# Performance work log

Measured on AMD Instinct MI355X. Metric: run time of the kernel, lower is better.

The kernel has to match this reference:

```python
import jax, jax.numpy as jnp
import numpy as np
import math

B, LA, LB, D, H = 8, 2048, 2048, 512, 512

def setup_inputs() -> dict:
    key = jax.random.key(0)
    ks = jax.random.split(key, 6)
    return {
        "input_a": jax.random.normal(ks[0], (B, LA, D), dtype=jnp.float32),
        "input_b": jax.random.normal(ks[1], (B, LB, D), dtype=jnp.float32),
        "mask_a": jax.random.randint(ks[2], (B, LA), 0, 2, dtype=jnp.int32),
        "mask_b": jax.random.randint(ks[3], (B, LB), 0, 2, dtype=jnp.int32),
        "Wa": jax.random.normal(ks[4], (D, H), dtype=jnp.float32) * (1.0 / math.sqrt(D)),
        "ba": jnp.zeros((H,), dtype=jnp.float32),
        "Wb": jax.random.normal(ks[5], (D, H), dtype=jnp.float32) * (1.0 / math.sqrt(D)),
        "bb": jnp.zeros((H,), dtype=jnp.float32),
    }

def reference(input_a, input_b, mask_a, mask_b, Wa, ba, Wb, bb):
    scale = 1.0 / math.sqrt(D)  # math.sqrt(input_dim_a)
    mapped_a = input_a @ Wa + ba            # [B, La, H]
    mapped_b = input_b @ Wb + bb            # [B, Lb, H]
    # final_mask = (mask_a outer mask_b) == 0
    final_mask = (mask_a[:, :, None] * mask_b[:, None, :]) == 0  # [B, La, Lb]
    scores = jnp.einsum('bih,bjh->bij', mapped_a, mapped_b) * scale
    scores = jnp.where(final_mask, jnp.float32(-1e9), scores)
    # attentions_a = softmax over Lb; attentions_b^T = softmax over La axis
    att_a = jax.nn.softmax(scores, axis=-1)   # [B, La, Lb]
    att_bT = jax.nn.softmax(scores, axis=1)   # [B, La, Lb] (= attentions_b.transpose(1,2))
    output_a = jnp.einsum('bij,bjd->bid', att_bT, input_b)  # [B, La, D]
    output_b = jnp.einsum('bij,bid->bjd', att_a, input_a)   # [B, Lb, D]
    return (output_a + input_a, output_b + input_b)
```

## Files before the change

kernel.cpp:

```cpp
#include <hip/hip_runtime.h>
#include <hip/hip_bf16.h>

#define BATCH 8
#define LSEQ 2048
#define DDIM 512

using f32x4 = __attribute__((ext_vector_type(4))) float;
using s16x8 = __attribute__((ext_vector_type(8))) short;

static __device__ __forceinline__ unsigned short f2b(float f) {
  __hip_bfloat16 h = __float2bfloat16(f);
  return __builtin_bit_cast(unsigned short, h);
}
static __device__ __forceinline__ float b2f(unsigned short u) {
  unsigned int v = ((unsigned int)u) << 16;
  return __builtin_bit_cast(float, v);
}

static __device__ __forceinline__ void gld16(const unsigned short* g, unsigned short* l) {
  __builtin_amdgcn_global_load_lds(
      (__attribute__((address_space(1))) void*)(g),
      (__attribute__((address_space(3))) void*)(l), 16, 0, 0);
}

__device__ __forceinline__ void mfma_kloop(
    const unsigned short* __restrict__ A, const unsigned short* __restrict__ Bt,
    int K, int lda, int ldb, unsigned short* sA, unsigned short* sB,
    int tid, f32x4 acc[4][4]) {
  const int wave = tid >> 6, lane = tid & 63;
  const int wm = (wave >> 1) * 64, wn = (wave & 1) * 64;
  const int lr = lane & 15, lq = lane >> 4;
  const int srow = tid >> 2;
  const int sk = (tid & 3) * 8;
  unsigned short* dA0 = sA + wave * 512;
  unsigned short* dA1 = sA + 2048 + wave * 512;
  unsigned short* dB0 = sB + wave * 512;
  unsigned short* dB1 = sB + 2048 + wave * 512;
  const unsigned short* pa0 = A + (size_t)srow * lda + sk;
  const unsigned short* pa1 = A + (size_t)(srow + 64) * lda + sk;
  const unsigned short* pb0 = Bt + (size_t)srow * ldb + sk;
  const unsigned short* pb1 = Bt + (size_t)(srow + 64) * ldb + sk;
  for (int k0 = 0; k0 < K; k0 += 32) {
    gld16(pa0 + k0, dA0);
    gld16(pa1 + k0, dA1);
    gld16(pb0 + k0, dB0);
    gld16(pb1 + k0, dB1);
    __syncthreads();
    s16x8 af[4], bf[4];
#pragma unroll
    for (int r = 0; r < 4; ++r)
      af[r] = *(const s16x8*)(sA + (wm + r * 16 + lr) * 32 + lq * 8);
#pragma unroll
    for (int c = 0; c < 4; ++c)
      bf[c] = *(const s16x8*)(sB + (wn + c * 16 + lr) * 32 + lq * 8);
#pragma unroll
    for (int r = 0; r < 4; ++r)
#pragma unroll
      for (int c = 0; c < 4; ++c)
        acc[r][c] = __builtin_amdgcn_mfma_f32_16x16x32_bf16(af[r], bf[c], acc[r][c], 0, 0, 0);
    __syncthreads();
  }
}

__global__ __launch_bounds__(256) void k_prep(const float* __restrict__ in_a,
                                              const float* __restrict__ in_b,
                                              const int* __restrict__ ma,
                                              const int* __restrict__ mb,
                                              unsigned short* __restrict__ oa,
                                              unsigned short* __restrict__ ob,
                                              float* __restrict__ Pa,
                                              float* __restrict__ Pb) {
  int z = blockIdx.z;
  const float* in = z ? in_b : in_a;
  const int* mask = z ? mb : ma;
  unsigned short* o16 = z ? ob : oa;
  float* partial = z ? Pb : Pa;
  int b = blockIdx.y;
  int l0 = blockIdx.x * 32;
  __shared__ int sm[32];
  if (threadIdx.x < 32) sm[threadIdx.x] = mask[b * LSEQ + l0 + threadIdx.x];
  __syncthreads();
  int d = threadIdx.x * 2;
  const float* base = in + ((size_t)b * LSEQ + l0) * DDIM + d;
  unsigned short* obase = o16 + ((size_t)b * LSEQ + l0) * DDIM + d;
  float ax = 0.f, ay = 0.f;
#pragma unroll 4
  for (int r = 0; r < 32; ++r) {
    float2 v = *(const float2*)(base + (size_t)r * DDIM);
    ushort2 u; u.x = f2b(v.x); u.y = f2b(v.y);
    *(ushort2*)(obase + (size_t)r * DDIM) = u;
    if (sm[r] == 0) { ax += v.x; ay += v.y; }
  }
  float2 o; o.x = ax; o.y = ay;
  *(float2*)(partial + ((size_t)(b * 64 + blockIdx.x)) * DDIM + d) = o;
}

__global__ __launch_bounds__(256) void k_p2(const float* __restrict__ Pa,
                                            const float* __restrict__ Pb,
                                            float* __restrict__ Ca,
                                            float* __restrict__ Cb) {
  int g = blockIdx.x;
  const float* src = (g < 8) ? Pa : Pb;
  float* dst = (g < 8) ? Ca : Cb;
  int b = g & 7;
  int d = threadIdx.x * 2;
  float ax = 0.f, ay = 0.f;
  for (int c = 0; c < 64; ++c) {
    float2 v = *(const float2*)(src + ((size_t)(b * 64 + c)) * DDIM + d);
    ax += v.x; ay += v.y;
  }
  dst[b * DDIM + d] = ax * (1.0f / LSEQ);
  dst[b * DDIM + d + 1] = ay * (1.0f / LSEQ);
}

__global__ __launch_bounds__(256) void k_transposeW(const float* __restrict__ Wa,
                                                    const float* __restrict__ Wb,
                                                    unsigned short* __restrict__ WaT,
                                                    unsigned short* __restrict__ WbT) {
  int gidx = blockIdx.x * 256 + threadIdx.x;
  const float* W = (gidx < 512 * 512) ? Wa : Wb;
  unsigned short* WT = (gidx < 512 * 512) ? WaT : WbT;
  int idx = gidx & (512 * 512 - 1);
  int h = idx >> 9, d = idx & 511;
  WT[idx] = f2b(W[d * DDIM + h]);
}

__global__ __launch_bounds__(256) void k_gemm_bias(const unsigned short* __restrict__ a16,
                                                   const unsigned short* __restrict__ b16,
                                                   const unsigned short* __restrict__ WaT,
                                                   const unsigned short* __restrict__ WbT,
                                                   const float* __restrict__ ba,
                                                   const float* __restrict__ bb,
                                                   unsigned short* __restrict__ mapa,
                                                   unsigned short* __restrict__ mapb) {
  int id = blockIdx.x;
  int g = id >> 5, rem = id & 31;
  int bn = (rem >> 3) * 128;
  int f = g * 8 + (rem & 7);
  int bm = (f & 127) * 128;
  int z = f >> 7;
  const unsigned short* A = z ? b16 : a16;
  const unsigned short* Bt = z ? WbT : WaT;
  const float* bias = z ? bb : ba;
  unsigned short* Cout = z ? mapb : mapa;
  __shared__ __align__(16) unsigned short sA[128 * 32], sB[128 * 32];
  f32x4 acc[4][4];
  f32x4 zero = {0.f, 0.f, 0.f, 0.f};
#pragma unroll
  for (int r = 0; r < 4; ++r)
#pragma unroll
    for (int c = 0; c < 4; ++c) acc[r][c] = zero;
  mfma_kloop(A + (size_t)bm * DDIM, Bt + (size_t)bn * DDIM, DDIM, DDIM, DDIM,
             sA, sB, threadIdx.x, acc);
  int wave = threadIdx.x >> 6, lane = threadIdx.x & 63;
  int wm = (wave >> 1) * 64, wn = (wave & 1) * 64, lr = lane & 15, lq = lane >> 4;
#pragma unroll
  for (int r = 0; r < 4; ++r)
#pragma unroll
    for (int c = 0; c < 4; ++c)
#pragma unroll
      for (int rr = 0; rr < 4; ++rr) {
        int row = bm + wm + r * 16 + lq * 4 + rr;
        int col = bn + wn + c * 16 + lr;
        Cout[(size_t)row * DDIM + col] = f2b(acc[r][c][rr] + bias[col]);
      }
}

__global__ __launch_bounds__(256) void k_scores(const unsigned short* __restrict__ mapa,
                                                const unsigned short* __restrict__ mapb,
                                                const int* __restrict__ mask_a,
                                                const int* __restrict__ mask_b,
                                                unsigned short* __restrict__ E,
                                                float* __restrict__ Zrow,
                                                float* __restrict__ Zcol) {
  int id = blockIdx.x;
  int low = id & 7, rest = id >> 3;
  int sub = rest & 15, Ghi = rest >> 4;
  int G = Ghi * 8 + low;
  int b = G >> 4, super = G & 15;
  int bi = (((super >> 2) << 2) + (sub >> 2)) * 128;
  int bj = (((super & 3) << 2) + (sub & 3)) * 128;
  __shared__ __align__(16) unsigned short sA[128 * 32], sB[128 * 32];
  __shared__ int sMa[128], sMb[128];
  int tid = threadIdx.x;
  if (tid < 128)
    sMa[tid] = mask_a[b * LSEQ + bi + tid];
  else
    sMb[tid - 128] = mask_b[b * LSEQ + bj + tid - 128];
  f32x4 acc[4][4];
  f32x4 zero = {0.f, 0.f, 0.f, 0.f};
#pragma unroll
  for (int r = 0; r < 4; ++r)
#pragma unroll
    for (int c = 0; c < 4; ++c) acc[r][c] = zero;
  mfma_kloop(mapa + ((size_t)b * LSEQ + bi) * DDIM, mapb + ((size_t)b * LSEQ + bj) * DDIM,
             DDIM, DDIM, DDIM, sA, sB, tid, acc);
  const float scale = 0.044194173824159216f;
  int wave = tid >> 6, lane = tid & 63;
  int wm = (wave >> 1) * 64, wn = (wave & 1) * 64, lr = lane & 15, lq = lane >> 4;
  unsigned short* Eb = E + (size_t)b * LSEQ * LSEQ + (size_t)bi * LSEQ + bj;
  float colp[4] = {0.f, 0.f, 0.f, 0.f};
  float rowp[4][4];
#pragma unroll
  for (int r = 0; r < 4; ++r) {
#pragma unroll
    for (int rr = 0; rr < 4; ++rr) rowp[r][rr] = 0.f;
#pragma unroll
    for (int c = 0; c < 4; ++c) {
      int jl = wn + c * 16 + lr;
      int mb_ = sMb[jl];
#pragma unroll
      for (int rr = 0; rr < 4; ++rr) {
        int il = wm + r * 16 + lq * 4 + rr;
        float e = (sMa[il] && mb_) ? __expf(acc[r][c][rr] * scale) : 0.f;
        rowp[r][rr] += e;
        colp[c] += e;
        Eb[(size_t)il * LSEQ + jl] = f2b(e);
      }
    }
  }
#pragma unroll
  for (int r = 0; r < 4; ++r)
#pragma unroll
    for (int rr = 0; rr < 4; ++rr) {
      float v = rowp[r][rr];
      v += __shfl_xor(v, 1);
      v += __shfl_xor(v, 2);
      v += __shfl_xor(v, 4);
      v += __shfl_xor(v, 8);
      if (lr == 0) {
        int il = wm + r * 16 + lq * 4 + rr;
        atomicAdd(&Zrow[b * LSEQ + bi + il], v);
      }
    }
#pragma unroll
  for (int c = 0; c < 4; ++c) {
    float v = colp[c];
    v += __shfl_xor(v, 16);
    v += __shfl_xor(v, 32);
    if (lq == 0) atomicAdd(&Zcol[b * LSEQ + bj + wn + c * 16 + lr], v);
  }
}

__global__ __launch_bounds__(256) void k_scaleT(const unsigned short* __restrict__ a16,
                                                const unsigned short* __restrict__ b16,
                                                const float* __restrict__ Zrow,
                                                const float* __restrict__ Zcol,
                                                unsigned short* __restrict__ atS,
                                                unsigned short* __restrict__ btS) {
  int zz = blockIdx.z;
  int b = zz & 7, sel = zz >> 3;
  const unsigned short* in = sel ? b16 : a16;
  const float* Z = sel ? Zcol : Zrow;
  unsigned short* out = sel ? btS : atS;
  int i0 = blockIdx.y * 64, d0 = blockIdx.x * 64;
  __shared__ unsigned short lt[64 * 65];
  __shared__ float zinv[64];
  if (threadIdx.x < 64) {
    float z = Z[b * LSEQ + i0 + threadIdx.x];
    zinv[threadIdx.x] = (z > 0.f) ? 1.f / z : 0.f;
  }
  __syncthreads();
  const unsigned short* ib = in + ((size_t)b * LSEQ + i0) * DDIM + d0;
#pragma unroll
  for (int p = 0; p < 16; ++p) {
    int idx = p * 256 + threadIdx.x;
    int dl = idx & 63, il = idx >> 6;
    lt[dl * 65 + il] = f2b(b2f(ib[(size_t)il * DDIM + dl]) * zinv[il]);
  }
  __syncthreads();
  unsigned short* ob = out + ((size_t)b * DDIM + d0) * LSEQ + i0;
#pragma unroll
  for (int p = 0; p < 16; ++p) {
    int idx = p * 256 + threadIdx.x;
    int il = idx & 63, dl = idx >> 6;
    ob[(size_t)dl * LSEQ + il] = lt[dl * 65 + il];
  }
}

__global__ __launch_bounds__(256) void k_gemm_outs(const unsigned short* __restrict__ E,
                                                   const unsigned short* __restrict__ btS,
                                                   const unsigned short* __restrict__ atS,
                                                   const unsigned short* __restrict__ a16,
                                                   const unsigned short* __restrict__ b16,
                                                   const float* __restrict__ Ca,
                                                   const float* __restrict__ Cb,
                                                   float* __restrict__ OutA,
                                                   float* __restrict__ OutB) {
  int id0 = blockIdx.x;
  int modeT = id0 >> 9;
  int id = id0 & 511;
  int g = id >> 5, rem = id & 31;
  int bn = (rem >> 3) * 128;
  int f = g * 8 + (rem & 7);
  int bm = (f & 15) * 128;
  int b = f >> 4;
  const unsigned short* Sop = modeT ? atS : btS;
  const unsigned short* addin = modeT ? b16 : a16;
  const float* Cvec = modeT ? Ca : Cb;
  float* Out = modeT ? OutB : OutA;

  __shared__ __align__(16) unsigned short sA[128 * 32], sB[128 * 32];
  int tid = threadIdx.x;
  const int wave = tid >> 6, lane = tid & 63;
  const int wm = (wave >> 1) * 64, wn = (wave & 1) * 64;
  const int lr = lane & 15, lq = lane >> 4;
  f32x4 acc[4][4];
  f32x4 zero = {0.f, 0.f, 0.f, 0.f};
#pragma unroll
  for (int r = 0; r < 4; ++r)
#pragma unroll
    for (int c = 0; c < 4; ++c) acc[r][c] = zero;

  if (!modeT) {
    mfma_kloop(E + (size_t)b * LSEQ * LSEQ + (size_t)bm * LSEQ,
               Sop + (size_t)b * DDIM * LSEQ + (size_t)bn * LSEQ,
               LSEQ, LSEQ, LSEQ, sA, sB, tid, acc);
  } else {
    const int srow = tid >> 2, sk = (tid & 3) * 8;
    unsigned short* dB0 = sB + wave * 512;
    unsigned short* dB1 = sB + 2048 + wave * 512;
    const unsigned short* Bb = Sop + (size_t)b * DDIM * LSEQ + (size_t)bn * LSEQ;
    const unsigned short* pb0 = Bb + (size_t)srow * LSEQ + sk;
    const unsigned short* pb1 = Bb + (size_t)(srow + 64) * LSEQ + sk;
    const int tc = tid & 15;
    const int tk = tc * 2;
    const int tm = (tid >> 4) * 8;
    const int gq = tc >> 2, wq = tc & 3;
    const unsigned short* pe = E + (size_t)b * LSEQ * LSEQ + (size_t)tk * LSEQ + bm + tm;
    for (int k0 = 0; k0 < LSEQ; k0 += 32) {
      gld16(pb0 + k0, dB0);
      gld16(pb1 + k0, dB1);
      uint4 e0 = *(const uint4*)(pe + (size_t)k0 * LSEQ);
      uint4 e1 = *(const uint4*)(pe + (size_t)k0 * LSEQ + LSEQ);
      unsigned short t0[8], t1[8];
      *(uint4*)t0 = e0; *(uint4*)t1 = e1;
#pragma unroll
      for (int j = 0; j < 8; ++j) {
        int row = tm + j;
        int sw = gq ^ ((row >> 3) & 3);
        unsigned int v = (unsigned int)t0[j] | ((unsigned int)t1[j] << 16);
        *(unsigned int*)(sA + row * 32 + sw * 8 + wq * 2) = v;
      }
      __syncthreads();
      s16x8 af[4], bf[4];
#pragma unroll
      for (int r = 0; r < 4; ++r) {
        int R = wm + r * 16 + lr;
        af[r] = *(const s16x8*)(sA + R * 32 + ((lq ^ ((R >> 3) & 3)) * 8));
      }
#pragma unroll
      for (int c = 0; c < 4; ++c)
        bf[c] = *(const s16x8*)(sB + (wn + c * 16 + lr) * 32 + lq * 8);
#pragma unroll
      for (int r = 0; r < 4; ++r)
#pragma unroll
        for (int c = 0; c < 4; ++c)
          acc[r][c] = __builtin_amdgcn_mfma_f32_16x16x32_bf16(af[r], bf[c], acc[r][c], 0, 0, 0);
      __syncthreads();
    }
  }

#pragma unroll
  for (int r = 0; r < 4; ++r)
#pragma unroll
    for (int c = 0; c < 4; ++c)
#pragma unroll
      for (int rr = 0; rr < 4; ++rr) {
        int row = bm + wm + r * 16 + lq * 4 + rr;
        int col = bn + wn + c * 16 + lr;
        size_t o = ((size_t)b * LSEQ + row) * DDIM + col;
        Out[o] = acc[r][c][rr] + b2f(addin[o]) + Cvec[b * DDIM + col];
      }
}

extern "C" void kernel_launch(void* const* d_in, const int* in_sizes, int n_in,
                              void* d_out, int out_size, void* d_ws, size_t ws_size,
                              hipStream_t stream) {
  (void)in_sizes; (void)n_in; (void)out_size; (void)ws_size;
  const float* in_a = (const float*)d_in[0];
  const float* in_b = (const float*)d_in[1];
  const int* ma = (const int*)d_in[2];
  const int* mb = (const int*)d_in[3];
  const float* Wa = (const float*)d_in[4];
  const float* ba = (const float*)d_in[5];
  const float* Wb = (const float*)d_in[6];
  const float* bb = (const float*)d_in[7];
  float* out = (float*)d_out;

  char* ws = (char*)d_ws;
  const size_t MB = 1ull << 20;
  unsigned short* a16 = (unsigned short*)(ws + 0 * MB);
  unsigned short* b16 = (unsigned short*)(ws + 16 * MB);
  unsigned short* WaT = (unsigned short*)(ws + 32 * MB);
  unsigned short* WbT = (unsigned short*)(ws + 32 * MB + 512 * 1024);
  unsigned short* mapa = (unsigned short*)(ws + 33 * MB);
  unsigned short* mapb = (unsigned short*)(ws + 49 * MB);
  unsigned short* E = (unsigned short*)(ws + 65 * MB);
  unsigned short* atS = (unsigned short*)(ws + 129 * MB);
  unsigned short* btS = (unsigned short*)(ws + 145 * MB);
  float* Zrow = (float*)(ws + 161 * MB);
  float* Zcol = (float*)(ws + 161 * MB + 65536);
  float* Ca = (float*)(ws + 161 * MB + 2 * 65536);
  float* Cb = (float*)(ws + 161 * MB + 2 * 65536 + 16384);
  float* Pa = (float*)(ws + 162 * MB);
  float* Pb = (float*)(ws + 163 * MB);

  hipMemsetAsync(Zrow, 0, 2 * 65536, stream);
  k_prep<<<dim3(64, 8, 2), 256, 0, stream>>>(in_a, in_b, ma, mb, a16, b16, Pa, Pb);
  k_transposeW<<<2048, 256, 0, stream>>>(Wa, Wb, WaT, WbT);
  k_p2<<<16, 256, 0, stream>>>(Pa, Pb, Ca, Cb);
  k_gemm_bias<<<1024, 256, 0, stream>>>(a16, b16, WaT, WbT, ba, bb, mapa, mapb);
  k_scores<<<2048, 256, 0, stream>>>(mapa, mapb, ma, mb, E, Zrow, Zcol);
  k_scaleT<<<dim3(8, 32, 16), 256, 0, stream>>>(a16, b16, Zrow, Zcol, atS, btS);
  k_gemm_outs<<<1024, 256, 0, stream>>>(E, btS, atS, a16, b16, Ca, Cb,
                                        out, out + (size_t)BATCH * LSEQ * DDIM);
}
```

Before: 365.7 us.

## Double-buffer LDS tiles in all MFMA GEMM loops to overlap loads with compute

Converts the shared K-loop and the transposed-E path to a two-stage LDS ping-pong: the next K-slice is issued via global_load_lds (and register loads for the transposed A tile) before the MFMAs on the current slice. This cuts one barrier per iteration and hides global latency behind matrix math. It doubles LDS per block (32KB), which may lower occupancy, and relies on explicit waitcnt plus s_barrier ordering.

```diff
diff --git a/kernel.cpp b/kernel.cpp
--- a/kernel.cpp
+++ b/kernel.cpp
@@ -23,7 +23,7 @@
       (__attribute__((address_space(3))) void*)(l), 16, 0, 0);
 }
 
-__device__ __forceinline__ void mfma_kloop(
+__device__ __forceinline__ void mfma_kloop2(
     const unsigned short* __restrict__ A, const unsigned short* __restrict__ Bt,
     int K, int lda, int ldb, unsigned short* sA, unsigned short* sB,
     int tid, f32x4 acc[4][4]) {
@@ -40,25 +40,39 @@
   const unsigned short* pa1 = A + (size_t)(srow + 64) * lda + sk;
   const unsigned short* pb0 = Bt + (size_t)srow * ldb + sk;
   const unsigned short* pb1 = Bt + (size_t)(srow + 64) * ldb + sk;
+  gld16(pa0, dA0);
+  gld16(pa1, dA1);
+  gld16(pb0, dB0);
+  gld16(pb1, dB1);
+  asm volatile("s_waitcnt vmcnt(0)" ::: "memory");
+  __builtin_amdgcn_s_barrier();
+  int cur = 0;
   for (int k0 = 0; k0 < K; k0 += 32) {
-    gld16(pa0 + k0, dA0);
-    gld16(pa1 + k0, dA1);
-    gld16(pb0 + k0, dB0);
-    gld16(pb1 + k0, dB1);
-    __syncthreads();
+    const int nxt = cur ^ 1;
+    if (k0 + 32 < K) {
+      const int off = nxt * 4096;
+      gld16(pa0 + k0 + 32, dA0 + off);
+      gld16(pa1 + k0 + 32, dA1 + off);
+      gld16(pb0 + k0 + 32, dB0 + off);
+      gld16(pb1 + k0 + 32, dB1 + off);
+    }
+    const unsigned short* cA = sA + cur * 4096;
+    const unsigned short* cB = sB + cur * 4096;
     s16x8 af[4], bf[4];
 #pragma unroll
     for (int r = 0; r < 4; ++r)
-      af[r] = *(const s16x8*)(sA + (wm + r * 16 + lr) * 32 + lq * 8);
+      af[r] = *(const s16x8*)(cA + (wm + r * 16 + lr) * 32 + lq * 8);
 #pragma unroll
     for (int c = 0; c < 4; ++c)
-      bf[c] = *(const s16x8*)(sB + (wn + c * 16 + lr) * 32 + lq * 8);
+      bf[c] = *(const s16x8*)(cB + (wn + c * 16 + lr) * 32 + lq * 8);
 #pragma unroll
     for (int r = 0; r < 4; ++r)
 #pragma unroll
       for (int c = 0; c < 4; ++c)
         acc[r][c] = __builtin_amdgcn_mfma_f32_16x16x32_bf16(af[r], bf[c], acc[r][c], 0, 0, 0);
-    __syncthreads();
+    asm volatile("s_waitcnt vmcnt(0)" ::: "memory");
+    __builtin_amdgcn_s_barrier();
+    cur = nxt;
   }
 }
 
@@ -143,15 +157,15 @@
   const unsigned short* Bt = z ? WbT : WaT;
   const float* bias = z ? bb : ba;
   unsigned short* Cout = z ? mapb : mapa;
-  __shared__ __align__(16) unsigned short sA[128 * 32], sB[128 * 32];
+  __shared__ __align__(16) unsigned short sA[2 * 128 * 32], sB[2 * 128 * 32];
   f32x4 acc[4][4];
   f32x4 zero = {0.f, 0.f, 0.f, 0.f};
 #pragma unroll
   for (int r = 0; r < 4; ++r)
 #pragma unroll
     for (int c = 0; c < 4; ++c) acc[r][c] = zero;
-  mfma_kloop(A + (size_t)bm * DDIM, Bt + (size_t)bn * DDIM, DDIM, DDIM, DDIM,
-             sA, sB, threadIdx.x, acc);
+  mfma_kloop2(A + (size_t)bm * DDIM, Bt + (size_t)bn * DDIM, DDIM, DDIM, DDIM,
+              sA, sB, threadIdx.x, acc);
   int wave = threadIdx.x >> 6, lane = threadIdx.x & 63;
   int wm = (wave >> 1) * 64, wn = (wave & 1) * 64, lr = lane & 15, lq = lane >> 4;
 #pragma unroll
@@ -180,21 +194,22 @@
   int b = G >> 4, super = G & 15;
   int bi = (((super >> 2) << 2) + (sub >> 2)) * 128;
   int bj = (((super & 3) << 2) + (sub & 3)) * 128;
-  __shared__ __align__(16) unsigned short sA[128 * 32], sB[128 * 32];
+  __shared__ __align__(16) unsigned short sA[2 * 128 * 32], sB[2 * 128 * 32];
   __shared__ int sMa[128], sMb[128];
   int tid = threadIdx.x;
   if (tid < 128)
     sMa[tid] = mask_a[b * LSEQ + bi + tid];
   else
     sMb[tid - 128] = mask_b[b * LSEQ + bj + tid - 128];
+  __syncthreads();
   f32x4 acc[4][4];
   f32x4 zero = {0.f, 0.f, 0.f, 0.f};
 #pragma unroll
   for (int r = 0; r < 4; ++r)
 #pragma unroll
     for (int c = 0; c < 4; ++c) acc[r][c] = zero;
-  mfma_kloop(mapa + ((size_t)b * LSEQ + bi) * DDIM, mapb + ((size_t)b * LSEQ + bj) * DDIM,
-             DDIM, DDIM, DDIM, sA, sB, tid, acc);
+  mfma_kloop2(mapa + ((size_t)b * LSEQ + bi) * DDIM, mapb + ((size_t)b * LSEQ + bj) * DDIM,
+              DDIM, DDIM, DDIM, sA, sB, tid, acc);
   const float scale = 0.044194173824159216f;
   int wave = tid >> 6, lane = tid & 63;
   int wm = (wave >> 1) * 64, wn = (wave & 1) * 64, lr = lane & 15, lq = lane >> 4;
@@ -300,7 +315,7 @@
   const float* Cvec = modeT ? Ca : Cb;
   float* Out = modeT ? OutB : OutA;
 
-  __shared__ __align__(16) unsigned short sA[128 * 32], sB[128 * 32];
+  __shared__ __align__(16) unsigned short sA[2 * 128 * 32], sB[2 * 128 * 32];
   int tid = threadIdx.x;
   const int wave = tid >> 6, lane = tid & 63;
   const int wm = (wave >> 1) * 64, wn = (wave & 1) * 64;
@@ -313,9 +328,9 @@
     for (int c = 0; c < 4; ++c) acc[r][c] = zero;
 
   if (!modeT) {
-    mfma_kloop(E + (size_t)b * LSEQ * LSEQ + (size_t)bm * LSEQ,
-               Sop + (size_t)b * DDIM * LSEQ + (size_t)bn * LSEQ,
-               LSEQ, LSEQ, LSEQ, sA, sB, tid, acc);
+    mfma_kloop2(E + (size_t)b * LSEQ * LSEQ + (size_t)bm * LSEQ,
+                Sop + (size_t)b * DDIM * LSEQ + (size_t)bn * LSEQ,
+                LSEQ, LSEQ, LSEQ, sA, sB, tid, acc);
   } else {
     const int srow = tid >> 2, sk = (tid & 3) * 8;
     unsigned short* dB0 = sB + wave * 512;
@@ -328,11 +343,12 @@
     const int tm = (tid >> 4) * 8;
     const int gq = tc >> 2, wq = tc & 3;
     const unsigned short* pe = E + (size_t)b * LSEQ * LSEQ + (size_t)tk * LSEQ + bm + tm;
-    for (int k0 = 0; k0 < LSEQ; k0 += 32) {
-      gld16(pb0 + k0, dB0);
-      gld16(pb1 + k0, dB1);
-      uint4 e0 = *(const uint4*)(pe + (size_t)k0 * LSEQ);
-      uint4 e1 = *(const uint4*)(pe + (size_t)k0 * LSEQ + LSEQ);
+
+    {
+      uint4 e0 = *(const uint4*)(pe);
+      uint4 e1 = *(const uint4*)(pe + LSEQ);
+      gld16(pb0, dB0);
+      gld16(pb1, dB1);
       unsigned short t0[8], t1[8];
       *(uint4*)t0 = e0; *(uint4*)t1 = e1;
 #pragma unroll
@@ -342,22 +358,51 @@
         unsigned int v = (unsigned int)t0[j] | ((unsigned int)t1[j] << 16);
         *(unsigned int*)(sA + row * 32 + sw * 8 + wq * 2) = v;
       }
-      __syncthreads();
+    }
+    asm volatile("s_waitcnt vmcnt(0) lgkmcnt(0)" ::: "memory");
+    __builtin_amdgcn_s_barrier();
+    int cur = 0;
+    for (int k0 = 0; k0 < LSEQ; k0 += 32) {
+      const int nxt = cur ^ 1;
+      const bool more = (k0 + 32 < LSEQ);
+      uint4 e0n = {0, 0, 0, 0}, e1n = {0, 0, 0, 0};
+      if (more) {
+        e0n = *(const uint4*)(pe + (size_t)(k0 + 32) * LSEQ);
+        e1n = *(const uint4*)(pe + (size_t)(k0 + 32) * LSEQ + LSEQ);
+        gld16(pb0 + k0 + 32, dB0 + nxt * 4096);
+        gld16(pb1 + k0 + 32, dB1 + nxt * 4096);
+      }
+      const unsigned short* cA = sA + cur * 4096;
+      const unsigned short* cB = sB + cur * 4096;
       s16x8 af[4], bf[4];
 #pragma unroll
       for (int r = 0; r < 4; ++r) {
         int R = wm + r * 16 + lr;
-        af[r] = *(const s16x8*)(sA + R * 32 + ((lq ^ ((R >> 3) & 3)) * 8));
+        af[r] = *(const s16x8*)(cA + R * 32 + ((lq ^ ((R >> 3) & 3)) * 8));
       }
 #pragma unroll
       for (int c = 0; c < 4; ++c)
-        bf[c] = *(const s16x8*)(sB + (wn + c * 16 + lr) * 32 + lq * 8);
+        bf[c] = *(const s16x8*)(cB + (wn + c * 16 + lr) * 32 + lq * 8);
 #pragma unroll
       for (int r = 0; r < 4; ++r)
 #pragma unroll
         for (int c = 0; c < 4; ++c)
           acc[r][c] = __builtin_amdgcn_mfma_f32_16x16x32_bf16(af[r], bf[c], acc[r][c], 0, 0, 0);
-      __syncthreads();
+      if (more) {
+        unsigned short t0[8], t1[8];
+        *(uint4*)t0 = e0n; *(uint4*)t1 = e1n;
+        unsigned short* nA = sA + nxt * 4096;
+#pragma unroll
+        for (int j = 0; j < 8; ++j) {
+          int row = tm + j;
+          int sw = gq ^ ((row >> 3) & 3);
+          unsigned int v = (unsigned int)t0[j] | ((unsigned int)t1[j] << 16);
+          *(unsigned int*)(nA + row * 32 + sw * 8 + wq * 2) = v;
+        }
+      }
+      asm volatile("s_waitcnt vmcnt(0) lgkmcnt(0)" ::: "memory");
+      __builtin_amdgcn_s_barrier();
+      cur = nxt;
     }
   }
 
```

Result: slower. 375.6 us (+2.7%).
